# Kernel tuning notes

Hardware: AMD Instinct MI355X
Metric: run time of the kernel (lower is better)

Reference implementation:

```python
import jax, jax.numpy as jnp
import numpy as np

EMB_DIM = 512
HIDDEN = 512
VOCAB = 50257
SEQ_LEN = 1024
IMG_H = 32
IMG_W = 32
ATTN_OUT = 64


def setup_inputs() -> dict:
    key = jax.random.key(0)
    ks = jax.random.split(key, 8)
    s_emb = 1.0 / np.sqrt(EMB_DIM)
    s_h = 1.0 / np.sqrt(HIDDEN)
    return {
        "instructions_batch": jax.random.randint(ks[0], (1, SEQ_LEN), 0, VOCAB, dtype=jnp.int64 if jax.config.jax_enable_x64 else jnp.int32),
        "emb_table": jax.random.normal(ks[1], (VOCAB, EMB_DIM), jnp.float32),
        "w_ih": jax.random.uniform(ks[2], (4 * HIDDEN, EMB_DIM), jnp.float32, -s_h, s_h),
        "w_hh": jax.random.uniform(ks[3], (4 * HIDDEN, HIDDEN), jnp.float32, -s_h, s_h),
        "b_ih": jax.random.uniform(ks[4], (4 * HIDDEN,), jnp.float32, -s_h, s_h),
        "b_hh": jax.random.uniform(ks[5], (4 * HIDDEN,), jnp.float32, -s_h, s_h),
        "attn_w": jax.random.uniform(ks[6], (ATTN_OUT, HIDDEN), jnp.float32, -s_emb, s_emb),
        "attn_b": jnp.zeros((ATTN_OUT,), jnp.float32),
    }


def _lstm_encode(tokens, emb_table, w_ih, w_hh, b_ih, b_hh):
    # tokens: [S] int; embeddings gathered once, then scan the recurrence.
    xs = emb_table[tokens]                      # [S, E]
    x_gates = xs @ w_ih.T + (b_ih + b_hh)       # [S, 4H] precompute input contribution

    def step(carry, xg):
        h, c = carry                            # [H], [H]
        gates = xg + h @ w_hh.T                 # [4H]
        i, f, g, o = jnp.split(gates, 4)
        i = jax.nn.sigmoid(i)
        f = jax.nn.sigmoid(f)
        g = jnp.tanh(g)
        o = jax.nn.sigmoid(o)
        c = f * c + i * g
        h = o * jnp.tanh(c)
        return (h, c), None

    h0 = jnp.zeros((HIDDEN,), xs.dtype)
    (h, _), _ = jax.lax.scan(step, (h0, h0), x_gates)
    return h                                     # [H]


def reference(instructions_batch, emb_table, w_ih, w_hh, b_ih, b_hh, attn_w, attn_b):
    h = _lstm_encode(instructions_batch[0], emb_table, w_ih, w_hh, b_ih, b_hh)
    x_instr_rep = h[None, :]                                    # [1, H]
    attn = jax.nn.sigmoid(x_instr_rep @ attn_w.T + attn_b)      # [1, 64]
    x_attention = jnp.broadcast_to(attn[:, :, None, None], (1, ATTN_OUT, IMG_H, IMG_W))
    return (x_attention, x_instr_rep)
```

## Files before the change

kernel.cpp:

```cpp
#include <hip/hip_runtime.h>
#include <hip/hip_bf16.h>
#include <math.h>

#define SEQ    1024
#define EMB    512
#define HID    512
#define G4     2048
#define NBLK   32
#define UPB    16
#define NSLOT  4

typedef unsigned long long u64;

__global__ __launch_bounds__(256) void xgates_kernel(
    const int* __restrict__ tok, const float* __restrict__ emb,
    const float* __restrict__ w_ih, const float* __restrict__ b_ih,
    const float* __restrict__ b_hh, float* __restrict__ xg)
{
  __shared__ float xs[64][68];
  __shared__ float wsh[64][68];
  __shared__ int   tok_s[64];

  const int tid = threadIdx.x;
  const int r0  = (int)blockIdx.x * 64;
  const int t0  = (int)blockIdx.y * 64;

  if (tid < 64) tok_s[tid] = tok[t0 + tid];
  __syncthreads();

  const int tx = tid & 15;
  const int ty = tid >> 4;

  float acc[4][4];
#pragma unroll
  for (int i = 0; i < 4; ++i)
#pragma unroll
    for (int j = 0; j < 4; ++j) acc[i][j] = 0.f;

  for (int kc = 0; kc < EMB; kc += 64) {
#pragma unroll
    for (int it = 0; it < 4; ++it) {
      int id  = it * 256 + tid;
      int row = id >> 4;
      int c4  = id & 15;
      float4 xv = *(const float4*)(emb + (size_t)tok_s[row] * EMB + kc + c4 * 4);
      *(float4*)&xs[row][c4 * 4] = xv;
      float4 wv = *(const float4*)(w_ih + (size_t)(r0 + row) * EMB + kc + c4 * 4);
      *(float4*)&wsh[row][c4 * 4] = wv;
    }
    __syncthreads();

#pragma unroll
    for (int k4 = 0; k4 < 16; ++k4) {
      float4 xv[4], wv[4];
#pragma unroll
      for (int i = 0; i < 4; ++i) xv[i] = *(const float4*)&xs[ty * 4 + i][k4 * 4];
#pragma unroll
      for (int j = 0; j < 4; ++j) wv[j] = *(const float4*)&wsh[tx * 4 + j][k4 * 4];
#pragma unroll
      for (int i = 0; i < 4; ++i)
#pragma unroll
        for (int j = 0; j < 4; ++j) {
          acc[i][j] += xv[i].x * wv[j].x + xv[i].y * wv[j].y
                     + xv[i].z * wv[j].z + xv[i].w * wv[j].w;
        }
    }
    __syncthreads();
  }

  const int rbase = r0 + tx * 4;
  float bias[4];
#pragma unroll
  for (int j = 0; j < 4; ++j) bias[j] = b_ih[rbase + j] + b_hh[rbase + j];

#pragma unroll
  for (int i = 0; i < 4; ++i) {
    int t = t0 + ty * 4 + i;
    float4 o;
    o.x = acc[i][0] + bias[0];
    o.y = acc[i][1] + bias[1];
    o.z = acc[i][2] + bias[2];
    o.w = acc[i][3] + bias[3];
    *(float4*)(xg + (size_t)t * G4 + rbase) = o;
  }
}

__global__ __launch_bounds__(512) void lstm_scan_kernel(
    const float* __restrict__ xg, const float* __restrict__ w_hh,
    u64* hslot )
{
  __shared__ float h_lds[512];
  __shared__ float part_lds[2][8 * 64];

  const int tid = threadIdx.x;
  const int blk = blockIdx.x;
  const int w   = tid >> 6;
  const int l   = tid & 63;
  const int q   = l >> 4;
  const int jj  = l & 15;
  const int grow = q * HID + blk * UPB + jj;

  float wreg[64];
  {
    const float* wp = w_hh + (size_t)grow * HID + w * 64;
#pragma unroll
    for (int k4 = 0; k4 < 16; ++k4) {
      float4 v = ((const float4*)wp)[k4];
      wreg[4 * k4 + 0] = v.x; wreg[4 * k4 + 1] = v.y;
      wreg[4 * k4 + 2] = v.z; wreg[4 * k4 + 3] = v.w;
    }
  }

  float c_reg = 0.f;
  float xgv = (w == 0) ? xg[grow] : 0.f;

  for (int t = 0; t < SEQ; ++t) {
    u64 word;
    const u64* src = hslot + (size_t)(t & (NSLOT - 1)) * HID + tid;
    do {
      word = __hip_atomic_load(src, __ATOMIC_RELAXED, __HIP_MEMORY_SCOPE_AGENT);
    } while ((unsigned)(word >> 32) != (unsigned)t);
    h_lds[tid] = __uint_as_float((unsigned)(word & 0xffffffffu));

    const float* hb = &h_lds[w * 64];
    float p0 = 0.f, p1 = 0.f, p2 = 0.f, p3 = 0.f;
#pragma unroll
    for (int k = 0; k < 16; ++k) {
      p0 += wreg[k]      * hb[k];
      p1 += wreg[k + 16] * hb[k + 16];
      p2 += wreg[k + 32] * hb[k + 32];
      p3 += wreg[k + 48] * hb[k + 48];
    }
    part_lds[t & 1][w * 64 + l] = (p0 + p1) + (p2 + p3);
    __syncthreads();

    if (w == 0) {
      const float* pp = &part_lds[t & 1][0];
      float s = ((pp[l]       + pp[64 + l]) + (pp[128 + l] + pp[192 + l]))
              + ((pp[256 + l] + pp[320 + l]) + (pp[384 + l] + pp[448 + l]));
      float gv = s + xgv;

      int tn = (t + 1 < SEQ) ? (t + 1) : (SEQ - 1);
      xgv = xg[(size_t)tn * G4 + grow];

      float gi = __shfl(gv, jj,      64);
      float gf = __shfl(gv, jj + 16, 64);
      float gg = __shfl(gv, jj + 32, 64);
      float go = __shfl(gv, jj + 48, 64);

      if (l < UPB) {
        const float LOG2E = 1.442695041f;
        float i_ = 1.f / (1.f + __builtin_exp2f(-LOG2E * gi));
        float f_ = 1.f / (1.f + __builtin_exp2f(-LOG2E * gf));
        float g_ = 2.f / (1.f + __builtin_exp2f(-2.f * LOG2E * gg)) - 1.f;
        float o_ = 1.f / (1.f + __builtin_exp2f(-LOG2E * go));
        c_reg = f_ * c_reg + i_ * g_;
        float hv = o_ * (2.f / (1.f + __builtin_exp2f(-2.f * LOG2E * c_reg)) - 1.f);
        u64 outw = ((u64)(unsigned)(t + 1) << 32) | (u64)__float_as_uint(hv);
        __hip_atomic_store(hslot + (size_t)((t + 1) & (NSLOT - 1)) * HID + blk * UPB + jj,
                           outw, __ATOMIC_RELAXED, __HIP_MEMORY_SCOPE_AGENT);
      }
    }
  }
}

__global__ __launch_bounds__(256) void head_kernel(
    const u64* __restrict__ hpacked, const float* __restrict__ attn_w,
    const float* __restrict__ attn_b, float* __restrict__ out)
{
  __shared__ float red[4];
  __shared__ float aval;
  const int r   = blockIdx.x;
  const int tid = threadIdx.x;

  float h0 = __uint_as_float((unsigned)(hpacked[tid]       & 0xffffffffu));
  float h1 = __uint_as_float((unsigned)(hpacked[256 + tid] & 0xffffffffu));

  float p = attn_w[(size_t)r * HID + tid] * h0
          + attn_w[(size_t)r * HID + 256 + tid] * h1;
#pragma unroll
  for (int off = 1; off < 64; off <<= 1) p += __shfl_xor(p, off, 64);
  if ((tid & 63) == 0) red[tid >> 6] = p;
  __syncthreads();
  if (tid == 0) {
    float sum = red[0] + red[1] + red[2] + red[3] + attn_b[r];
    aval = 1.f / (1.f + __expf(-sum));
  }
  __syncthreads();

  float a = aval;
  float4 av = make_float4(a, a, a, a);
  ((float4*)(out + (size_t)r * 1024))[tid] = av;

  if (r == 0) {
    out[65536 + tid]       = h0;
    out[65536 + 256 + tid] = h1;
  }
}

extern "C" void kernel_launch(void* const* d_in, const int* in_sizes, int n_in,
                              void* d_out, int out_size, void* d_ws, size_t ws_size,
                              hipStream_t stream) {
  const int*   tok    = (const int*)  d_in[0];
  const float* emb    = (const float*)d_in[1];
  const float* w_ih   = (const float*)d_in[2];
  const float* w_hh   = (const float*)d_in[3];
  const float* b_ih   = (const float*)d_in[4];
  const float* b_hh   = (const float*)d_in[5];
  const float* attn_w = (const float*)d_in[6];
  const float* attn_b = (const float*)d_in[7];
  float* out = (float*)d_out;

  char* ws = (char*)d_ws;
  float* xg    = (float*)ws;
  u64*   hslot = (u64*)(ws + (size_t)SEQ * G4 * 4);

  hipMemsetAsync(hslot, 0, NSLOT * HID * sizeof(u64), stream);

  dim3 gA(G4 / 64, SEQ / 64);
  xgates_kernel<<<gA, 256, 0, stream>>>(tok, emb, w_ih, b_ih, b_hh, xg);
  lstm_scan_kernel<<<NBLK, 512, 0, stream>>>(xg, w_hh, hslot);
  head_kernel<<<64, 256, 0, stream>>>(hslot, attn_w, attn_b, out);
}
```

Baseline: 1.765 ms.

## Fuse input-gate GEMM, LSTM scan and head into one persistent kernel

Merges the three kernels into a single launch. Helper blocks compute the x-gate GEMM in 32-timestep chunks and publish per-chunk ready counters, and the 32 scan blocks spin on those counters so the recurrence can start before the whole GEMM finishes. The scan blocks then compute the attention head themselves, which removes two kernel launches. The risks are deadlock if the scan blocks are not co-resident with the helpers, and helper blocks competing with the latency-bound scan for memory bandwidth.

```diff
diff --git a/kernel.cpp b/kernel.cpp
--- a/kernel.cpp
+++ b/kernel.cpp
@@ -6,98 +6,89 @@
 #define EMB    512
 #define HID    512
 #define G4     2048
-#define NBLK   32
+#define NSCAN  32
+#define NHELP  224
 #define UPB    16
 #define NSLOT  4
 
 typedef unsigned long long u64;
 
-__global__ __launch_bounds__(256) void xgates_kernel(
+__global__ __launch_bounds__(512) void fused_kernel(
     const int* __restrict__ tok, const float* __restrict__ emb,
-    const float* __restrict__ w_ih, const float* __restrict__ b_ih,
-    const float* __restrict__ b_hh, float* __restrict__ xg)
+    const float* __restrict__ w_ih, const float* __restrict__ w_hh,
+    const float* __restrict__ b_ih, const float* __restrict__ b_hh,
+    const float* __restrict__ attn_w, const float* __restrict__ attn_b,
+    float* __restrict__ out,
+    float* __restrict__ xg, u64* hslot, int* rdy32)
 {
-  __shared__ float xs[64][68];
+  __shared__ float xs[32][68];
   __shared__ float wsh[64][68];
-  __shared__ int   tok_s[64];
-
-  const int tid = threadIdx.x;
-  const int r0  = (int)blockIdx.x * 64;
-  const int t0  = (int)blockIdx.y * 64;
-
-  if (tid < 64) tok_s[tid] = tok[t0 + tid];
-  __syncthreads();
-
-  const int tx = tid & 15;
-  const int ty = tid >> 4;
-
-  float acc[4][4];
-#pragma unroll
-  for (int i = 0; i < 4; ++i)
-#pragma unroll
-    for (int j = 0; j < 4; ++j) acc[i][j] = 0.f;
-
-  for (int kc = 0; kc < EMB; kc += 64) {
-#pragma unroll
-    for (int it = 0; it < 4; ++it) {
-      int id  = it * 256 + tid;
-      int row = id >> 4;
-      int c4  = id & 15;
-      float4 xv = *(const float4*)(emb + (size_t)tok_s[row] * EMB + kc + c4 * 4);
-      *(float4*)&xs[row][c4 * 4] = xv;
-      float4 wv = *(const float4*)(w_ih + (size_t)(r0 + row) * EMB + kc + c4 * 4);
-      *(float4*)&wsh[row][c4 * 4] = wv;
-    }
-    __syncthreads();
-
-#pragma unroll
-    for (int k4 = 0; k4 < 16; ++k4) {
-      float4 xv[4], wv[4];
-#pragma unroll
-      for (int i = 0; i < 4; ++i) xv[i] = *(const float4*)&xs[ty * 4 + i][k4 * 4];
-#pragma unroll
-      for (int j = 0; j < 4; ++j) wv[j] = *(const float4*)&wsh[tx * 4 + j][k4 * 4];
-#pragma unroll
-      for (int i = 0; i < 4; ++i)
-#pragma unroll
-        for (int j = 0; j < 4; ++j) {
-          acc[i][j] += xv[i].x * wv[j].x + xv[i].y * wv[j].y
-                     + xv[i].z * wv[j].z + xv[i].w * wv[j].w;
-        }
-    }
-    __syncthreads();
-  }
-
-  const int rbase = r0 + tx * 4;
-  float bias[4];
-#pragma unroll
-  for (int j = 0; j < 4; ++j) bias[j] = b_ih[rbase + j] + b_hh[rbase + j];
-
-#pragma unroll
-  for (int i = 0; i < 4; ++i) {
-    int t = t0 + ty * 4 + i;
-    float4 o;
-    o.x = acc[i][0] + bias[0];
-    o.y = acc[i][1] + bias[1];
-    o.z = acc[i][2] + bias[2];
-    o.w = acc[i][3] + bias[3];
-    *(float4*)(xg + (size_t)t * G4 + rbase) = o;
-  }
-}
-
-__global__ __launch_bounds__(512) void lstm_scan_kernel(
-    const float* __restrict__ xg, const float* __restrict__ w_hh,
-    u64* hslot )
-{
+  __shared__ int   tok_s[32];
   __shared__ float h_lds[512];
-  __shared__ float part_lds[2][8 * 64];
+  __shared__ float part_lds[2][512];
+  __shared__ float redh[8];
+  __shared__ float avals[2];
 
   const int tid = threadIdx.x;
   const int blk = blockIdx.x;
-  const int w   = tid >> 6;
-  const int l   = tid & 63;
-  const int q   = l >> 4;
-  const int jj  = l & 15;
+
+  if (blk >= NSCAN) {
+    const int hb = blk - NSCAN;
+    const int tx = tid & 31;
+    const int ty = tid >> 5;
+    for (int tau = hb; tau < 1024; tau += NHELP) {
+      const int t0 = (tau >> 5) * 32;
+      const int r0 = (tau & 31) * 64;
+      if (tid < 32) tok_s[tid] = tok[t0 + tid];
+      __syncthreads();
+
+      float a00 = 0.f, a01 = 0.f, a10 = 0.f, a11 = 0.f;
+      for (int kc = 0; kc < EMB; kc += 64) {
+        {
+          int row = tid >> 4, c4 = tid & 15;
+          *(float4*)&xs[row][c4 * 4] =
+              *(const float4*)(emb + (size_t)tok_s[row] * EMB + kc + c4 * 4);
+        }
+#pragma unroll
+        for (int it = 0; it < 2; ++it) {
+          int id = it * 512 + tid;
+          int row = id >> 4, c4 = id & 15;
+          *(float4*)&wsh[row][c4 * 4] =
+              *(const float4*)(w_ih + (size_t)(r0 + row) * EMB + kc + c4 * 4);
+        }
+        __syncthreads();
+#pragma unroll
+        for (int k4 = 0; k4 < 16; ++k4) {
+          float4 x0 = *(const float4*)&xs[ty * 2 + 0][k4 * 4];
+          float4 x1 = *(const float4*)&xs[ty * 2 + 1][k4 * 4];
+          float4 w0 = *(const float4*)&wsh[tx * 2 + 0][k4 * 4];
+          float4 w1 = *(const float4*)&wsh[tx * 2 + 1][k4 * 4];
+          a00 += x0.x * w0.x + x0.y * w0.y + x0.z * w0.z + x0.w * w0.w;
+          a01 += x0.x * w1.x + x0.y * w1.y + x0.z * w1.z + x0.w * w1.w;
+          a10 += x1.x * w0.x + x1.y * w0.y + x1.z * w0.z + x1.w * w0.w;
+          a11 += x1.x * w1.x + x1.y * w1.y + x1.z * w1.z + x1.w * w1.w;
+        }
+        __syncthreads();
+      }
+      const int rb = r0 + tx * 2;
+      float b0 = b_ih[rb]     + b_hh[rb];
+      float b1 = b_ih[rb + 1] + b_hh[rb + 1];
+      float2 o0 = make_float2(a00 + b0, a01 + b1);
+      float2 o1 = make_float2(a10 + b0, a11 + b1);
+      *(float2*)(xg + (size_t)(t0 + ty * 2)     * G4 + rb) = o0;
+      *(float2*)(xg + (size_t)(t0 + ty * 2 + 1) * G4 + rb) = o1;
+
+      __threadfence();
+      __syncthreads();
+      if (tid == 0) atomicAdd(&rdy32[tau >> 5], 1);
+    }
+    return;
+  }
+
+  const int w  = tid >> 6;
+  const int l  = tid & 63;
+  const int q  = l >> 4;
+  const int jj = l & 15;
   const int grow = q * HID + blk * UPB + jj;
 
   float wreg[64];
@@ -112,7 +103,15 @@
   }
 
   float c_reg = 0.f;
-  float xgv = (w == 0) ? xg[grow] : 0.f;
+  float xgv = 0.f;
+  int known = 0;
+  if (w == 0) {
+    while (__hip_atomic_load(&rdy32[0], __ATOMIC_RELAXED,
+                             __HIP_MEMORY_SCOPE_AGENT) < 32) { }
+    __threadfence();
+    known = 1;
+    xgv = xg[grow];
+  }
 
   for (int t = 0; t < SEQ; ++t) {
     u64 word;
@@ -136,11 +135,18 @@
 
     if (w == 0) {
       const float* pp = &part_lds[t & 1][0];
-      float s = ((pp[l]       + pp[64 + l]) + (pp[128 + l] + pp[192 + l]))
+      float s = ((pp[l]       + pp[64 + l])  + (pp[128 + l] + pp[192 + l]))
               + ((pp[256 + l] + pp[320 + l]) + (pp[384 + l] + pp[448 + l]));
       float gv = s + xgv;
 
       int tn = (t + 1 < SEQ) ? (t + 1) : (SEQ - 1);
+      int nc = tn >> 5;
+      if (nc >= known) {
+        while (__hip_atomic_load(&rdy32[nc], __ATOMIC_RELAXED,
+                                 __HIP_MEMORY_SCOPE_AGENT) < 32) { }
+        __threadfence();
+        known = nc + 1;
+      }
       xgv = xg[(size_t)tn * G4 + grow];
 
       float gi = __shfl(gv, jj,      64);
@@ -162,39 +168,37 @@
       }
     }
   }
-}
-
-__global__ __launch_bounds__(256) void head_kernel(
-    const u64* __restrict__ hpacked, const float* __restrict__ attn_w,
-    const float* __restrict__ attn_b, float* __restrict__ out)
-{
-  __shared__ float red[4];
-  __shared__ float aval;
-  const int r   = blockIdx.x;
-  const int tid = threadIdx.x;
-
-  float h0 = __uint_as_float((unsigned)(hpacked[tid]       & 0xffffffffu));
-  float h1 = __uint_as_float((unsigned)(hpacked[256 + tid] & 0xffffffffu));
-
-  float p = attn_w[(size_t)r * HID + tid] * h0
-          + attn_w[(size_t)r * HID + 256 + tid] * h1;
-#pragma unroll
-  for (int off = 1; off < 64; off <<= 1) p += __shfl_xor(p, off, 64);
-  if ((tid & 63) == 0) red[tid >> 6] = p;
-  __syncthreads();
-  if (tid == 0) {
-    float sum = red[0] + red[1] + red[2] + red[3] + attn_b[r];
-    aval = 1.f / (1.f + __expf(-sum));
-  }
-  __syncthreads();
-
-  float a = aval;
-  float4 av = make_float4(a, a, a, a);
-  ((float4*)(out + (size_t)r * 1024))[tid] = av;
-
-  if (r == 0) {
-    out[65536 + tid]       = h0;
-    out[65536 + 256 + tid] = h1;
+
+  {
+    const u64* src = hslot + tid;
+    u64 word;
+    do {
+      word = __hip_atomic_load(src, __ATOMIC_RELAXED, __HIP_MEMORY_SCOPE_AGENT);
+    } while ((unsigned)(word >> 32) != (unsigned)SEQ);
+    h_lds[tid] = __uint_as_float((unsigned)(word & 0xffffffffu));
+    __syncthreads();
+
+    const int vw   = tid >> 6;
+    const int rsel = vw >> 2;
+    const int row  = blk * 2 + rsel;
+    const int k    = tid & 255;
+
+    float p = attn_w[(size_t)row * HID + k]       * h_lds[k]
+            + attn_w[(size_t)row * HID + 256 + k] * h_lds[256 + k];
+#pragma unroll
+    for (int off = 1; off < 64; off <<= 1) p += __shfl_xor(p, off, 64);
+    if ((tid & 63) == 0) redh[vw] = p;
+    __syncthreads();
+    if (tid < 2) {
+      float sum = redh[tid * 4] + redh[tid * 4 + 1]
+                + redh[tid * 4 + 2] + redh[tid * 4 + 3] + attn_b[blk * 2 + tid];
+      avals[tid] = 1.f / (1.f + __expf(-sum));
+    }
+    __syncthreads();
+
+    float a = avals[rsel];
+    ((float4*)(out + (size_t)row * 1024))[k] = make_float4(a, a, a, a);
+    if (blk == 0) out[65536 + tid] = h_lds[tid];
   }
 }
 
@@ -214,11 +218,10 @@
   char* ws = (char*)d_ws;
   float* xg    = (float*)ws;
   u64*   hslot = (u64*)(ws + (size_t)SEQ * G4 * 4);
-
-  hipMemsetAsync(hslot, 0, NSLOT * HID * sizeof(u64), stream);
-
-  dim3 gA(G4 / 64, SEQ / 64);
-  xgates_kernel<<<gA, 256, 0, stream>>>(tok, emb, w_ih, b_ih, b_hh, xg);
-  lstm_scan_kernel<<<NBLK, 512, 0, stream>>>(xg, w_hh, hslot);
-  head_kernel<<<64, 256, 0, stream>>>(hslot, attn_w, attn_b, out);
+  int*   rdy32 = (int*)(ws + (size_t)SEQ * G4 * 4 + NSLOT * HID * sizeof(u64));
+
+  hipMemsetAsync(hslot, 0, NSLOT * HID * sizeof(u64) + 32 * sizeof(int), stream);
+
+  fused_kernel<<<NSCAN + NHELP, 512, 0, stream>>>(
+      tok, emb, w_ih, w_hh, b_ih, b_hh, attn_w, attn_b, out, xg, hslot, rdy32);
 }
```

Result: slower. 1.831 ms (+3.8%).

## Halve scan blocks with two gate rows per thread and fuse attention head

Applied to the files above, without the earlier changes.

Cuts the persistent LSTM scan grid from 32 to 16 blocks, each owning 32 hidden units. Every thread now holds two rows of W_hh in registers and reads h with float4 loads. The cross-wave reduction is spread over all eight waves instead of only wave 0, and the swizzled LDS indices are meant to avoid bank conflicts. The attention head kernel is folded into the scan kernel's epilogue to remove one launch. This lowers the number of blocks that must see each step's h through the global flag handshake, at the cost of doubling register pressure (128 weight floats per thread) and more per-block work on each step.

```diff
diff --git a/kernel.cpp b/kernel.cpp
--- a/kernel.cpp
+++ b/kernel.cpp
@@ -6,8 +6,8 @@
 #define EMB    512
 #define HID    512
 #define G4     2048
-#define NBLK   32
-#define UPB    16
+#define NSCAN  16
+#define UPB    32
 #define NSLOT  4
 
 typedef unsigned long long u64;
@@ -43,10 +43,10 @@
       int id  = it * 256 + tid;
       int row = id >> 4;
       int c4  = id & 15;
-      float4 xv = *(const float4*)(emb + (size_t)tok_s[row] * EMB + kc + c4 * 4);
-      *(float4*)&xs[row][c4 * 4] = xv;
-      float4 wv = *(const float4*)(w_ih + (size_t)(r0 + row) * EMB + kc + c4 * 4);
-      *(float4*)&wsh[row][c4 * 4] = wv;
+      *(float4*)&xs[row][c4 * 4] =
+          *(const float4*)(emb + (size_t)tok_s[row] * EMB + kc + c4 * 4);
+      *(float4*)&wsh[row][c4 * 4] =
+          *(const float4*)(w_ih + (size_t)(r0 + row) * EMB + kc + c4 * 4);
     }
     __syncthreads();
 
@@ -87,114 +87,133 @@
 
 __global__ __launch_bounds__(512) void lstm_scan_kernel(
     const float* __restrict__ xg, const float* __restrict__ w_hh,
-    u64* hslot )
+    const float* __restrict__ attn_w, const float* __restrict__ attn_b,
+    float* __restrict__ out, u64* hslot)
 {
   __shared__ float h_lds[512];
-  __shared__ float part_lds[2][8 * 64];
+  __shared__ float pl[2][1024];
+  __shared__ float redh[8];
+  __shared__ float avals[4];
 
   const int tid = threadIdx.x;
-  const int blk = blockIdx.x;
+  const int b   = blockIdx.x;
   const int w   = tid >> 6;
   const int l   = tid & 63;
-  const int q   = l >> 4;
-  const int jj  = l & 15;
-  const int grow = q * HID + blk * UPB + jj;
-
-  float wreg[64];
+  const int u   = l & 31;
+  const int qh  = l >> 5;
+  const int R0 = qh * HID + b * UPB + u;
+  const int R1 = (2 + qh) * HID + b * UPB + u;
+  const int wr0 = w * 128 + qh * 32       + ((u + 8 * qh) & 31);
+  const int wr1 = w * 128 + (qh + 2) * 32 + ((u + 8 * (qh + 2)) & 31);
+
+  const int qr  = l & 3;
+  const int Ur  = 4 * w + (l >> 2);
+  const int xrow = qr * HID + b * UPB + Ur;
+  const int rcol = qr * 32 + ((Ur + 8 * qr) & 31);
+
+  float w0r[64], w1r[64];
   {
-    const float* wp = w_hh + (size_t)grow * HID + w * 64;
+    const float4* p0 = (const float4*)(w_hh + (size_t)R0 * HID + w * 64);
+    const float4* p1 = (const float4*)(w_hh + (size_t)R1 * HID + w * 64);
 #pragma unroll
     for (int k4 = 0; k4 < 16; ++k4) {
-      float4 v = ((const float4*)wp)[k4];
-      wreg[4 * k4 + 0] = v.x; wreg[4 * k4 + 1] = v.y;
-      wreg[4 * k4 + 2] = v.z; wreg[4 * k4 + 3] = v.w;
+      float4 a = p0[k4], c = p1[k4];
+      w0r[4 * k4 + 0] = a.x; w0r[4 * k4 + 1] = a.y;
+      w0r[4 * k4 + 2] = a.z; w0r[4 * k4 + 3] = a.w;
+      w1r[4 * k4 + 0] = c.x; w1r[4 * k4 + 1] = c.y;
+      w1r[4 * k4 + 2] = c.z; w1r[4 * k4 + 3] = c.w;
     }
   }
 
   float c_reg = 0.f;
-  float xgv = (w == 0) ? xg[grow] : 0.f;
+  float xqv = (l < 16) ? xg[xrow] : 0.f;
 
   for (int t = 0; t < SEQ; ++t) {
+    const u64* src = hslot + (size_t)(t & (NSLOT - 1)) * HID + tid;
     u64 word;
-    const u64* src = hslot + (size_t)(t & (NSLOT - 1)) * HID + tid;
     do {
       word = __hip_atomic_load(src, __ATOMIC_RELAXED, __HIP_MEMORY_SCOPE_AGENT);
     } while ((unsigned)(word >> 32) != (unsigned)t);
-    h_lds[tid] = __uint_as_float((unsigned)(word & 0xffffffffu));
+    h_lds[tid] = __uint_as_float((unsigned)word);
 
     const float* hb = &h_lds[w * 64];
-    float p0 = 0.f, p1 = 0.f, p2 = 0.f, p3 = 0.f;
-#pragma unroll
-    for (int k = 0; k < 16; ++k) {
-      p0 += wreg[k]      * hb[k];
-      p1 += wreg[k + 16] * hb[k + 16];
-      p2 += wreg[k + 32] * hb[k + 32];
-      p3 += wreg[k + 48] * hb[k + 48];
-    }
-    part_lds[t & 1][w * 64 + l] = (p0 + p1) + (p2 + p3);
-    __syncthreads();
-
-    if (w == 0) {
-      const float* pp = &part_lds[t & 1][0];
-      float s = ((pp[l]       + pp[64 + l]) + (pp[128 + l] + pp[192 + l]))
-              + ((pp[256 + l] + pp[320 + l]) + (pp[384 + l] + pp[448 + l]));
-      float gv = s + xgv;
-
+    float p0 = 0.f, p1 = 0.f, q0 = 0.f, q1 = 0.f;
+#pragma unroll
+    for (int k4 = 0; k4 < 16; ++k4) {
+      float4 hv = *(const float4*)&hb[k4 * 4];
+      p0 += w0r[4 * k4 + 0] * hv.x + w0r[4 * k4 + 1] * hv.y;
+      p1 += w0r[4 * k4 + 2] * hv.z + w0r[4 * k4 + 3] * hv.w;
+      q0 += w1r[4 * k4 + 0] * hv.x + w1r[4 * k4 + 1] * hv.y;
+      q1 += w1r[4 * k4 + 2] * hv.z + w1r[4 * k4 + 3] * hv.w;
+    }
+    float* pc = pl[t & 1];
+    pc[wr0] = p0 + p1;
+    pc[wr1] = q0 + q1;
+    __syncthreads();
+
+    float gv = 0.f;
+    if (l < 16) {
+      const float* pp = pl[t & 1];
+      float s0 = pp[0 * 128 + rcol] + pp[1 * 128 + rcol];
+      float s1 = pp[2 * 128 + rcol] + pp[3 * 128 + rcol];
+      float s2 = pp[4 * 128 + rcol] + pp[5 * 128 + rcol];
+      float s3 = pp[6 * 128 + rcol] + pp[7 * 128 + rcol];
+      gv = (s0 + s1) + (s2 + s3) + xqv;
       int tn = (t + 1 < SEQ) ? (t + 1) : (SEQ - 1);
-      xgv = xg[(size_t)tn * G4 + grow];
-
-      float gi = __shfl(gv, jj,      64);
-      float gf = __shfl(gv, jj + 16, 64);
-      float gg = __shfl(gv, jj + 32, 64);
-      float go = __shfl(gv, jj + 48, 64);
-
-      if (l < UPB) {
-        const float LOG2E = 1.442695041f;
-        float i_ = 1.f / (1.f + __builtin_exp2f(-LOG2E * gi));
-        float f_ = 1.f / (1.f + __builtin_exp2f(-LOG2E * gf));
-        float g_ = 2.f / (1.f + __builtin_exp2f(-2.f * LOG2E * gg)) - 1.f;
-        float o_ = 1.f / (1.f + __builtin_exp2f(-LOG2E * go));
-        c_reg = f_ * c_reg + i_ * g_;
-        float hv = o_ * (2.f / (1.f + __builtin_exp2f(-2.f * LOG2E * c_reg)) - 1.f);
-        u64 outw = ((u64)(unsigned)(t + 1) << 32) | (u64)__float_as_uint(hv);
-        __hip_atomic_store(hslot + (size_t)((t + 1) & (NSLOT - 1)) * HID + blk * UPB + jj,
-                           outw, __ATOMIC_RELAXED, __HIP_MEMORY_SCOPE_AGENT);
-      }
-    }
-  }
-}
-
-__global__ __launch_bounds__(256) void head_kernel(
-    const u64* __restrict__ hpacked, const float* __restrict__ attn_w,
-    const float* __restrict__ attn_b, float* __restrict__ out)
-{
-  __shared__ float red[4];
-  __shared__ float aval;
-  const int r   = blockIdx.x;
-  const int tid = threadIdx.x;
-
-  float h0 = __uint_as_float((unsigned)(hpacked[tid]       & 0xffffffffu));
-  float h1 = __uint_as_float((unsigned)(hpacked[256 + tid] & 0xffffffffu));
-
-  float p = attn_w[(size_t)r * HID + tid] * h0
-          + attn_w[(size_t)r * HID + 256 + tid] * h1;
-#pragma unroll
-  for (int off = 1; off < 64; off <<= 1) p += __shfl_xor(p, off, 64);
-  if ((tid & 63) == 0) red[tid >> 6] = p;
-  __syncthreads();
-  if (tid == 0) {
-    float sum = red[0] + red[1] + red[2] + red[3] + attn_b[r];
-    aval = 1.f / (1.f + __expf(-sum));
-  }
-  __syncthreads();
-
-  float a = aval;
-  float4 av = make_float4(a, a, a, a);
-  ((float4*)(out + (size_t)r * 1024))[tid] = av;
-
-  if (r == 0) {
-    out[65536 + tid]       = h0;
-    out[65536 + 256 + tid] = h1;
+      xqv = xg[(size_t)tn * G4 + xrow];
+    }
+    float gi = __shfl(gv, 4 * (l & 3) + 0, 64);
+    float gf = __shfl(gv, 4 * (l & 3) + 1, 64);
+    float gg = __shfl(gv, 4 * (l & 3) + 2, 64);
+    float go = __shfl(gv, 4 * (l & 3) + 3, 64);
+
+    if (l < 4) {
+      const float LOG2E = 1.442695041f;
+      float i_ = 1.f / (1.f + __builtin_exp2f(-LOG2E * gi));
+      float f_ = 1.f / (1.f + __builtin_exp2f(-LOG2E * gf));
+      float g_ = 2.f / (1.f + __builtin_exp2f(-2.f * LOG2E * gg)) - 1.f;
+      float o_ = 1.f / (1.f + __builtin_exp2f(-LOG2E * go));
+      c_reg = f_ * c_reg + i_ * g_;
+      float hv = o_ * (2.f / (1.f + __builtin_exp2f(-2.f * LOG2E * c_reg)) - 1.f);
+      u64 outw = ((u64)(unsigned)(t + 1) << 32) | (u64)__float_as_uint(hv);
+      __hip_atomic_store(
+          hslot + (size_t)((t + 1) & (NSLOT - 1)) * HID + b * UPB + 4 * w + l,
+          outw, __ATOMIC_RELAXED, __HIP_MEMORY_SCOPE_AGENT);
+    }
+  }
+
+  {
+    const u64* src = hslot + tid;
+    u64 word;
+    do {
+      word = __hip_atomic_load(src, __ATOMIC_RELAXED, __HIP_MEMORY_SCOPE_AGENT);
+    } while ((unsigned)(word >> 32) != (unsigned)SEQ);
+    h_lds[tid] = __uint_as_float((unsigned)word);
+    __syncthreads();
+
+    const int row  = 4 * b + (w & 3);
+    const int half = w >> 2;
+    const int k0   = half * 256 + l * 4;
+    float4 wv = *(const float4*)(attn_w + (size_t)row * HID + k0);
+    float4 hv = *(const float4*)&h_lds[k0];
+    float p = wv.x * hv.x + wv.y * hv.y + wv.z * hv.z + wv.w * hv.w;
+#pragma unroll
+    for (int off = 1; off < 64; off <<= 1) p += __shfl_xor(p, off, 64);
+    if (l == 0) redh[w] = p;
+    __syncthreads();
+    if (tid < 4) {
+      float s = redh[tid] + redh[tid + 4] + attn_b[4 * b + tid];
+      avals[tid] = 1.f / (1.f + __expf(-s));
+    }
+    __syncthreads();
+
+    const int rr = tid >> 7, kk = tid & 127;
+    float a = avals[rr];
+    float4 av = make_float4(a, a, a, a);
+    float4* op = (float4*)(out + (size_t)(4 * b + rr) * 1024);
+    op[kk * 2]     = av;
+    op[kk * 2 + 1] = av;
+    if (b == 0) out[65536 + tid] = h_lds[tid];
   }
 }
 
@@ -211,14 +230,12 @@
   const float* attn_b = (const float*)d_in[7];
   float* out = (float*)d_out;
 
-  char* ws = (char*)d_ws;
-  float* xg    = (float*)ws;
-  u64*   hslot = (u64*)(ws + (size_t)SEQ * G4 * 4);
+  float* xg    = (float*)d_ws;
+  u64*   hslot = (u64*)((char*)d_ws + (size_t)SEQ * G4 * 4);
 
   hipMemsetAsync(hslot, 0, NSLOT * HID * sizeof(u64), stream);
 
   dim3 gA(G4 / 64, SEQ / 64);
   xgates_kernel<<<gA, 256, 0, stream>>>(tok, emb, w_ih, b_ih, b_hh, xg);
-  lstm_scan_kernel<<<NBLK, 512, 0, stream>>>(xg, w_hh, hslot);
-  head_kernel<<<64, 256, 0, stream>>>(hslot, attn_w, attn_b, out);
+  lstm_scan_kernel<<<NSCAN, 512, 0, stream>>>(xg, w_hh, attn_w, attn_b, out, hslot);
 }
```

Result: slower. 2.582 ms (+46.3%).
